# Kernel tuning notes

Measured on AMD Instinct MI355X. Metric: run time of the kernel, lower is better.

## Reference

```python
import jax, jax.numpy as jnp
import numpy as np

H = 128      # hidden_size
P = 50000    # num_predicates
C = 20000    # num_clauses
K = 3        # clause_size (3-SAT)
B = 4        # batch
SAT_ITERS = 2


def setup_inputs() -> dict:
    key = jax.random.key(0)
    ks = jax.random.split(key, 10)
    s = 0.02
    return {
        "clause_indices": jax.random.randint(ks[0], (B, C, K), 0, P),
        "variable_states": jax.random.normal(ks[1], (B, P, H), jnp.float32),
        "W_vc": jax.random.normal(ks[2], (H, H), jnp.float32) * s,
        "b_vc": jnp.zeros((H,), jnp.float32),
        "W_ce": jax.random.normal(ks[3], (H, H), jnp.float32) * s,
        "b_ce": jnp.zeros((H,), jnp.float32),
        "W_cv": jax.random.normal(ks[4], (H, H), jnp.float32) * s,
        "b_cv": jnp.zeros((H,), jnp.float32),
        "W_s1": jax.random.normal(ks[5], (H, H), jnp.float32) * s,
        "b_s1": jnp.zeros((H,), jnp.float32),
        "W_s2": jax.random.normal(ks[6], (1, H), jnp.float32) * s,
        "b_s2": jnp.zeros((1,), jnp.float32),
    }


def _forward(clause_indices, variable_states,
             W_vc, b_vc, W_ce, b_ce, W_cv, b_cv, W_s1, b_s1, W_s2, b_s2):
    Bn, Cn, Kn = clause_indices.shape
    Pn = variable_states.shape[1]
    # first-occurrence mask within each clause: duplicates of a variable inside
    # one clause must contribute once ((clause_indices == v).any(-1) semantics).
    eq = clause_indices[..., :, None] == clause_indices[..., None, :]  # [B,C,K,K]
    first = ~jnp.any(jnp.tril(eq, -1), axis=-1)                        # [B,C,K]
    w = first.reshape(-1).astype(variable_states.dtype)                # [B*C*K]
    flat_idx = clause_indices.reshape(-1)                              # [B*C*K]
    counts = jax.ops.segment_sum(w, flat_idx, num_segments=Pn)        # [P]
    batch_ix = jnp.arange(Bn)[:, None, None]

    for _ in range(SAT_ITERS):
        # clause side: gather -> var_to_clause -> mean over clause -> clause_embedding
        gathered = variable_states[batch_ix, clause_indices]           # [B,C,K,H]
        cv = jnp.einsum('bckh,oh->bcko', gathered, W_vc) + b_vc        # [B,C,K,H]
        clause_states = jnp.einsum('bch,oh->bco', cv.mean(2), W_ce) + b_ce  # [B,C,H]
        # variable side: per-variable mean of clause_to_var over all (b, c)
        # where the variable appears; message broadcast across batch.
        M = jnp.einsum('bch,oh->bco', clause_states, W_cv) + b_cv      # [B,C,H]
        Mflat = jnp.broadcast_to(M[:, :, None, :], (Bn, Cn, Kn, M.shape[-1])).reshape(-1, M.shape[-1])
        sums = jax.ops.segment_sum(Mflat * w[:, None], flat_idx, num_segments=Pn)  # [P,H]
        msgs = jnp.where(counts[:, None] > 0,
                         sums / jnp.maximum(counts, 1.0)[:, None],
                         0.0)                                          # [P,H]
        variable_states = variable_states + msgs[None]                 # broadcast over batch

    h = jax.nn.relu(jnp.einsum('bph,oh->bpo', variable_states, W_s1) + b_s1)
    logits = jnp.einsum('bph,oh->bpo', h, W_s2) + b_s2                 # [B,P,1]
    return jax.nn.sigmoid(logits)[..., 0]                              # [B,P]


def reference(clause_indices, variable_states,
              W_vc, b_vc, W_ce, b_ce, W_cv, b_cv, W_s1, b_s1, W_s2, b_s2):
    return _forward(clause_indices, variable_states,
                    W_vc, b_vc, W_ce, b_ce, W_cv, b_cv, W_s1, b_s1, W_s2, b_s2)
```

## Files before the change

kernel.cpp:

```cpp
#include <hip/hip_runtime.h>
#include <math.h>

using u16 = unsigned short;
using u32 = unsigned int;

namespace {
constexpr int Hdim = 128;
constexpr int Pn = 50000;
constexpr int Cn = 20000;
constexpr int Bn = 4;
constexpr int NClause = Bn * Cn;
constexpr int NRows = Bn * Pn;
constexpr int CAP = 64;
}

typedef __attribute__((ext_vector_type(4))) float f32x4;
typedef __attribute__((ext_vector_type(8))) short bf16x8;

static __device__ __forceinline__ float bf2f(u16 v) {
    u32 u = ((u32)v) << 16;
    return __builtin_bit_cast(float, u);
}
static __device__ __forceinline__ u16 f2bf(float f) {
    u32 u = __builtin_bit_cast(u32, f);
    u32 r = u + 0x7FFFu + ((u >> 16) & 1u);
    return (u16)(r >> 16);
}

__global__ __launch_bounds__(128) void setup_kernel(
    const float* __restrict__ W_vc, const float* __restrict__ b_vc,
    const float* __restrict__ W_ce, const float* __restrict__ b_ce,
    const float* __restrict__ W_cv, const float* __restrict__ b_cv,
    const float* __restrict__ W_s1,
    u16* __restrict__ WcombPack, u16* __restrict__ Ws1Pack,
    float* __restrict__ bias_comb, int* __restrict__ cursor) {
    int o = blockIdx.x, t = threadIdx.x;
    __shared__ float u[Hdim];
    __shared__ float red[Hdim];
    float acc = 0.f;
#pragma unroll 8
    for (int h = 0; h < Hdim; ++h) acc = fmaf(W_cv[o * Hdim + h], W_ce[h * Hdim + t], acc);
    u[t] = acc;
    float b1 = b_ce[t];
#pragma unroll 8
    for (int h = 0; h < Hdim; ++h) b1 = fmaf(W_ce[t * Hdim + h], b_vc[h], b1);
    red[t] = W_cv[o * Hdim + t] * b1;
    __syncthreads();
#pragma unroll
    for (int s = 64; s > 0; s >>= 1) {
        if (t < s) red[t] += red[t + s];
        __syncthreads();
    }
    if (t == 0) bias_comb[o] = red[0] + b_cv[o];
    float w = 0.f;
#pragma unroll 8
    for (int h = 0; h < Hdim; ++h) w = fmaf(u[h], W_vc[h * Hdim + t], w);
    int nt = o >> 4, ks = t >> 5, lofs = (t >> 3) & 3, j = t & 7;
    int lane = lofs * 16 + (o & 15);
    size_t dst = (size_t)(((nt * 4 + ks) * 64 + lane)) * 8 + j;
    WcombPack[dst] = f2bf(w);
    Ws1Pack[dst] = f2bf(W_s1[o * Hdim + t]);
    for (int i = o * 128 + t; i < Pn; i += 128 * 128) cursor[i] = 0;
}

__global__ void fill_kernel(const int* __restrict__ ci, int* __restrict__ cursor,
                            int* __restrict__ entries) {
    int fid = blockIdx.x * blockDim.x + threadIdx.x;
    if (fid >= NClause) return;
    int i0 = ci[fid * 3 + 0], i1 = ci[fid * 3 + 1], i2 = ci[fid * 3 + 2];
    int pos = atomicAdd(&cursor[i0], 1);
    entries[i0 * CAP + pos] = fid;
    if (i1 != i0) { pos = atomicAdd(&cursor[i1], 1); entries[i1 * CAP + pos] = fid; }
    if (i2 != i0 && i2 != i1) { pos = atomicAdd(&cursor[i2], 1); entries[i2 * CAP + pos] = fid; }
}

template <int FROM_F32>
__global__ __launch_bounds__(256) void clause_kernel(
    const int* __restrict__ ci, const float* __restrict__ vs0, const u16* __restrict__ msgs,
    const u16* __restrict__ Bpack, const float* __restrict__ bias, u16* __restrict__ M) {
    __shared__ __align__(16) u16 Atile[64 * 136];
    __shared__ __align__(16) u16 Btile[128 * 128];
    int tid = threadIdx.x;
    int block0 = blockIdx.x * 64;
    {
        const bf16x8* s = (const bf16x8*)Bpack;
        bf16x8* d = (bf16x8*)Btile;
#pragma unroll
        for (int i = 0; i < 8; ++i) d[tid + i * 256] = s[tid + i * 256];
    }
#pragma unroll
    for (int pass = 0; pass < 4; ++pass) {
        int t = pass * 256 + tid;
        int r = t >> 4, seg = t & 15;
        int fid = block0 + r;
        int i0 = ci[fid * 3 + 0], i1 = ci[fid * 3 + 1], i2 = ci[fid * 3 + 2];
        int co = seg * 8;
        float s[8];
        if (FROM_F32) {
            const float* base = vs0 + (size_t)(fid / Cn) * Pn * Hdim;
            const float* r0 = base + (size_t)i0 * Hdim + co;
            const float* r1 = base + (size_t)i1 * Hdim + co;
            const float* r2 = base + (size_t)i2 * Hdim + co;
            f32x4 a0 = *(const f32x4*)r0, a1 = *(const f32x4*)(r0 + 4);
            f32x4 b0 = *(const f32x4*)r1, b1 = *(const f32x4*)(r1 + 4);
            f32x4 c0 = *(const f32x4*)r2, c1 = *(const f32x4*)(r2 + 4);
#pragma unroll
            for (int j = 0; j < 4; ++j) {
                s[j] = a0[j] + b0[j] + c0[j];
                s[j + 4] = a1[j] + b1[j] + c1[j];
            }
        } else {
            bf16x8 v0 = *(const bf16x8*)(msgs + (size_t)i0 * Hdim + co);
            bf16x8 v1 = *(const bf16x8*)(msgs + (size_t)i1 * Hdim + co);
            bf16x8 v2 = *(const bf16x8*)(msgs + (size_t)i2 * Hdim + co);
#pragma unroll
            for (int j = 0; j < 8; ++j)
                s[j] = bf2f((u16)v0[j]) + bf2f((u16)v1[j]) + bf2f((u16)v2[j]);
        }
        bf16x8 o;
#pragma unroll
        for (int j = 0; j < 8; ++j) o[j] = (short)f2bf(s[j] * (1.f / 3.f));
        *(bf16x8*)(&Atile[r * 136 + seg * 8]) = o;
    }
    __syncthreads();
    int w = tid >> 6, l = tid & 63;
    int arow = w * 16 + (l & 15);
    int kofs = (l >> 4) * 8;
    f32x4 acc[8];
#pragma unroll
    for (int nt = 0; nt < 8; ++nt) acc[nt] = (f32x4){0.f, 0.f, 0.f, 0.f};
#pragma unroll
    for (int ks = 0; ks < 4; ++ks) {
        bf16x8 af = *(const bf16x8*)(&Atile[arow * 136 + ks * 32 + kofs]);
#pragma unroll
        for (int nt = 0; nt < 8; ++nt) {
            bf16x8 bfr = *(const bf16x8*)(&Btile[((nt * 4 + ks) * 64 + l) * 8]);
            acc[nt] = __builtin_amdgcn_mfma_f32_16x16x32_bf16(af, bfr, acc[nt], 0, 0, 0);
        }
    }
    __syncthreads();
    int crow = w * 16 + (l >> 4) * 4;
#pragma unroll
    for (int nt = 0; nt < 8; ++nt) {
        int col = nt * 16 + (l & 15);
        float bc = FROM_F32 ? bias[col] : 0.f;
#pragma unroll
        for (int reg = 0; reg < 4; ++reg)
            Atile[(crow + reg) * 136 + col] = f2bf(acc[nt][reg] + bc);
    }
    __syncthreads();
#pragma unroll
    for (int pass = 0; pass < 4; ++pass) {
        int t = pass * 256 + tid;
        int r = t >> 4, seg = t & 15;
        *(bf16x8*)(M + (size_t)(block0 + r) * Hdim + seg * 8) =
            *(const bf16x8*)(&Atile[r * 136 + seg * 8]);
    }
}

__global__ __launch_bounds__(256) void var_kernel(const u16* __restrict__ M,
                                                  const int* __restrict__ counts,
                                                  const int* __restrict__ entries,
                                                  u16* __restrict__ msgs, int iter2) {
    int wave = threadIdx.x >> 6, lane = threadIdx.x & 63;
    int p = blockIdx.x * 4 + wave;
    if (p >= Pn) return;
    int deg = counts[p];
    const int* ep = entries + p * CAP;
    float a0 = 0.f, a1 = 0.f;
    for (int e = 0; e < deg; ++e) {
        int cid = ep[e];
        u32 v = *(const u32*)(M + (size_t)cid * Hdim + lane * 2);
        a0 += bf2f((u16)(v & 0xffffu));
        a1 += bf2f((u16)(v >> 16));
    }
    if (deg > 0) { float inv = 1.f / (float)deg; a0 *= inv; a1 *= inv; }
    u32* mp = (u32*)(msgs + (size_t)p * Hdim + lane * 2);
    if (iter2) {
        u32 old = *mp;
        a0 += 2.f * bf2f((u16)(old & 0xffffu));
        a1 += 2.f * bf2f((u16)(old >> 16));
    }
    *mp = (u32)f2bf(a0) | ((u32)f2bf(a1) << 16);
}

__global__ __launch_bounds__(256) void final_kernel(
    const float* __restrict__ vs0, const u16* __restrict__ msgs, const u16* __restrict__ Bpack,
    const float* __restrict__ b_s1, const float* __restrict__ W_s2, const float* __restrict__ b_s2,
    float* __restrict__ out) {
    __shared__ __align__(16) u16 Atile[64 * 136];
    __shared__ __align__(16) u16 Btile[128 * 128];
    int tid = threadIdx.x;
    int block0 = blockIdx.x * 64;
    {
        const bf16x8* s = (const bf16x8*)Bpack;
        bf16x8* d = (bf16x8*)Btile;
#pragma unroll
        for (int i = 0; i < 8; ++i) d[tid + i * 256] = s[tid + i * 256];
    }
#pragma unroll
    for (int pass = 0; pass < 4; ++pass) {
        int t = pass * 256 + tid;
        int r = t >> 4, seg = t & 15;
        int row = block0 + r;
        int p = row % Pn;
        int co = seg * 8;
        const float* vp = vs0 + (size_t)row * Hdim + co;
        f32x4 x = *(const f32x4*)vp, y = *(const f32x4*)(vp + 4);
        bf16x8 m = *(const bf16x8*)(msgs + (size_t)p * Hdim + co);
        bf16x8 o;
#pragma unroll
        for (int j = 0; j < 4; ++j) {
            o[j] = (short)f2bf(x[j] + bf2f((u16)m[j]));
            o[j + 4] = (short)f2bf(y[j] + bf2f((u16)m[j + 4]));
        }
        *(bf16x8*)(&Atile[r * 136 + seg * 8]) = o;
    }
    __syncthreads();
    int w = tid >> 6, l = tid & 63;
    int arow = w * 16 + (l & 15);
    int kofs = (l >> 4) * 8;
    f32x4 acc[8];
#pragma unroll
    for (int nt = 0; nt < 8; ++nt) acc[nt] = (f32x4){0.f, 0.f, 0.f, 0.f};
#pragma unroll
    for (int ks = 0; ks < 4; ++ks) {
        bf16x8 af = *(const bf16x8*)(&Atile[arow * 136 + ks * 32 + kofs]);
#pragma unroll
        for (int nt = 0; nt < 8; ++nt) {
            bf16x8 bfr = *(const bf16x8*)(&Btile[((nt * 4 + ks) * 64 + l) * 8]);
            acc[nt] = __builtin_amdgcn_mfma_f32_16x16x32_bf16(af, bfr, acc[nt], 0, 0, 0);
        }
    }
    float part[4] = {0.f, 0.f, 0.f, 0.f};
#pragma unroll
    for (int nt = 0; nt < 8; ++nt) {
        int col = nt * 16 + (l & 15);
        float b1 = b_s1[col], w2 = W_s2[col];
#pragma unroll
        for (int reg = 0; reg < 4; ++reg)
            part[reg] += fmaxf(acc[nt][reg] + b1, 0.f) * w2;
    }
#pragma unroll
    for (int m = 1; m < 16; m <<= 1)
#pragma unroll
        for (int reg = 0; reg < 4; ++reg) part[reg] += __shfl_xor(part[reg], m, 64);
    if ((l & 15) == 0) {
        float lb = b_s2[0];
        int row0 = block0 + w * 16 + (l >> 4) * 4;
#pragma unroll
        for (int reg = 0; reg < 4; ++reg)
            out[row0 + reg] = 1.f / (1.f + expf(-(part[reg] + lb)));
    }
}

extern "C" void kernel_launch(void* const* d_in, const int* in_sizes, int n_in,
                              void* d_out, int out_size, void* d_ws, size_t ws_size,
                              hipStream_t stream) {
    (void)in_sizes; (void)n_in; (void)out_size; (void)ws_size;
    const int* ci = (const int*)d_in[0];
    const float* vs0 = (const float*)d_in[1];
    const float* W_vc = (const float*)d_in[2];
    const float* b_vc = (const float*)d_in[3];
    const float* W_ce = (const float*)d_in[4];
    const float* b_ce = (const float*)d_in[5];
    const float* W_cv = (const float*)d_in[6];
    const float* b_cv = (const float*)d_in[7];
    const float* W_s1 = (const float*)d_in[8];
    const float* b_s1 = (const float*)d_in[9];
    const float* W_s2 = (const float*)d_in[10];
    const float* b_s2 = (const float*)d_in[11];
    float* out = (float*)d_out;

    char* ws = (char*)d_ws;
    size_t off = 0;
    auto alloc = [&](size_t bytes) -> void* {
        off = (off + 255) & ~(size_t)255;
        void* p = ws + off;
        off += bytes;
        return p;
    };
    float* bias_comb = (float*)alloc(Hdim * 4);
    u16* WcombPack = (u16*)alloc(Hdim * Hdim * 2);
    u16* Ws1Pack = (u16*)alloc(Hdim * Hdim * 2);
    int* cursor = (int*)alloc(Pn * 4);
    int* entries = (int*)alloc((size_t)Pn * CAP * 4);
    u16* M = (u16*)alloc((size_t)NClause * Hdim * 2);
    u16* msgs = (u16*)alloc((size_t)Pn * Hdim * 2);

    setup_kernel<<<Hdim, Hdim, 0, stream>>>(W_vc, b_vc, W_ce, b_ce, W_cv, b_cv, W_s1,
                                            WcombPack, Ws1Pack, bias_comb, cursor);
    fill_kernel<<<(NClause + 255) / 256, 256, 0, stream>>>(ci, cursor, entries);

    clause_kernel<1><<<NClause / 64, 256, 0, stream>>>(ci, vs0, nullptr, WcombPack, bias_comb, M);
    var_kernel<<<(Pn + 3) / 4, 256, 0, stream>>>(M, cursor, entries, msgs, 0);
    clause_kernel<0><<<NClause / 64, 256, 0, stream>>>(ci, nullptr, msgs, WcombPack, bias_comb, M);
    var_kernel<<<(Pn + 3) / 4, 256, 0, stream>>>(M, cursor, entries, msgs, 1);
    final_kernel<<<NRows / 64, 256, 0, stream>>>(vs0, msgs, Ws1Pack, b_s1, W_s2, b_s2, out);
}
```

Baseline: 159.5 us.

## Fuse adjacency fill into first clause kernel, unroll var gather, persistent final kernel

Removes the separate fill_kernel by building the variable-to-clause adjacency lists inside the first clause kernel, using the first 64 threads of each block. The var_kernel gather loop is unrolled by two with separate accumulators so more loads are in flight at once. The final kernel becomes a grid-stride persistent kernel with 768 blocks, so the 128x128 weight tile is loaded into shared memory once per block instead of once per 64-row tile. These trade one fewer launch and less redundant weight loading for extra atomic work in the clause kernel and extra syncs per tile in the final kernel.

```diff
diff --git a/kernel.cpp b/kernel.cpp
--- a/kernel.cpp
+++ b/kernel.cpp
@@ -63,21 +63,11 @@
     for (int i = o * 128 + t; i < Pn; i += 128 * 128) cursor[i] = 0;
 }
 
-__global__ void fill_kernel(const int* __restrict__ ci, int* __restrict__ cursor,
-                            int* __restrict__ entries) {
-    int fid = blockIdx.x * blockDim.x + threadIdx.x;
-    if (fid >= NClause) return;
-    int i0 = ci[fid * 3 + 0], i1 = ci[fid * 3 + 1], i2 = ci[fid * 3 + 2];
-    int pos = atomicAdd(&cursor[i0], 1);
-    entries[i0 * CAP + pos] = fid;
-    if (i1 != i0) { pos = atomicAdd(&cursor[i1], 1); entries[i1 * CAP + pos] = fid; }
-    if (i2 != i0 && i2 != i1) { pos = atomicAdd(&cursor[i2], 1); entries[i2 * CAP + pos] = fid; }
-}
-
-template <int FROM_F32>
+template <int FROM_F32, int DO_FILL>
 __global__ __launch_bounds__(256) void clause_kernel(
     const int* __restrict__ ci, const float* __restrict__ vs0, const u16* __restrict__ msgs,
-    const u16* __restrict__ Bpack, const float* __restrict__ bias, u16* __restrict__ M) {
+    const u16* __restrict__ Bpack, const float* __restrict__ bias, u16* __restrict__ M,
+    int* __restrict__ cursor, int* __restrict__ entries) {
     __shared__ __align__(16) u16 Atile[64 * 136];
     __shared__ __align__(16) u16 Btile[128 * 128];
     int tid = threadIdx.x;
@@ -87,6 +77,14 @@
         bf16x8* d = (bf16x8*)Btile;
 #pragma unroll
         for (int i = 0; i < 8; ++i) d[tid + i * 256] = s[tid + i * 256];
+    }
+    if (DO_FILL && tid < 64) {
+        int fid = block0 + tid;
+        int i0 = ci[fid * 3 + 0], i1 = ci[fid * 3 + 1], i2 = ci[fid * 3 + 2];
+        int pos = atomicAdd(&cursor[i0], 1);
+        entries[i0 * CAP + pos] = fid;
+        if (i1 != i0) { pos = atomicAdd(&cursor[i1], 1); entries[i1 * CAP + pos] = fid; }
+        if (i2 != i0 && i2 != i1) { pos = atomicAdd(&cursor[i2], 1); entries[i2 * CAP + pos] = fid; }
     }
 #pragma unroll
     for (int pass = 0; pass < 4; ++pass) {
@@ -167,13 +165,23 @@
     if (p >= Pn) return;
     int deg = counts[p];
     const int* ep = entries + p * CAP;
-    float a0 = 0.f, a1 = 0.f;
-    for (int e = 0; e < deg; ++e) {
-        int cid = ep[e];
-        u32 v = *(const u32*)(M + (size_t)cid * Hdim + lane * 2);
+    float a0 = 0.f, a1 = 0.f, c0 = 0.f, c1 = 0.f;
+    int e = 0;
+    for (; e + 1 < deg; e += 2) {
+        int cidA = ep[e], cidB = ep[e + 1];
+        u32 vA = *(const u32*)(M + (size_t)cidA * Hdim + lane * 2);
+        u32 vB = *(const u32*)(M + (size_t)cidB * Hdim + lane * 2);
+        a0 += bf2f((u16)(vA & 0xffffu));
+        a1 += bf2f((u16)(vA >> 16));
+        c0 += bf2f((u16)(vB & 0xffffu));
+        c1 += bf2f((u16)(vB >> 16));
+    }
+    if (e < deg) {
+        u32 v = *(const u32*)(M + (size_t)ep[e] * Hdim + lane * 2);
         a0 += bf2f((u16)(v & 0xffffu));
         a1 += bf2f((u16)(v >> 16));
     }
+    a0 += c0; a1 += c1;
     if (deg > 0) { float inv = 1.f / (float)deg; a0 *= inv; a1 *= inv; }
     u32* mp = (u32*)(msgs + (size_t)p * Hdim + lane * 2);
     if (iter2) {
@@ -187,70 +195,73 @@
 __global__ __launch_bounds__(256) void final_kernel(
     const float* __restrict__ vs0, const u16* __restrict__ msgs, const u16* __restrict__ Bpack,
     const float* __restrict__ b_s1, const float* __restrict__ W_s2, const float* __restrict__ b_s2,
-    float* __restrict__ out) {
+    float* __restrict__ out, int ntiles) {
     __shared__ __align__(16) u16 Atile[64 * 136];
     __shared__ __align__(16) u16 Btile[128 * 128];
     int tid = threadIdx.x;
-    int block0 = blockIdx.x * 64;
     {
         const bf16x8* s = (const bf16x8*)Bpack;
         bf16x8* d = (bf16x8*)Btile;
 #pragma unroll
         for (int i = 0; i < 8; ++i) d[tid + i * 256] = s[tid + i * 256];
     }
-#pragma unroll
-    for (int pass = 0; pass < 4; ++pass) {
-        int t = pass * 256 + tid;
-        int r = t >> 4, seg = t & 15;
-        int row = block0 + r;
-        int p = row % Pn;
-        int co = seg * 8;
-        const float* vp = vs0 + (size_t)row * Hdim + co;
-        f32x4 x = *(const f32x4*)vp, y = *(const f32x4*)(vp + 4);
-        bf16x8 m = *(const bf16x8*)(msgs + (size_t)p * Hdim + co);
-        bf16x8 o;
-#pragma unroll
-        for (int j = 0; j < 4; ++j) {
-            o[j] = (short)f2bf(x[j] + bf2f((u16)m[j]));
-            o[j + 4] = (short)f2bf(y[j] + bf2f((u16)m[j + 4]));
-        }
-        *(bf16x8*)(&Atile[r * 136 + seg * 8]) = o;
-    }
-    __syncthreads();
     int w = tid >> 6, l = tid & 63;
     int arow = w * 16 + (l & 15);
     int kofs = (l >> 4) * 8;
-    f32x4 acc[8];
-#pragma unroll
-    for (int nt = 0; nt < 8; ++nt) acc[nt] = (f32x4){0.f, 0.f, 0.f, 0.f};
-#pragma unroll
-    for (int ks = 0; ks < 4; ++ks) {
-        bf16x8 af = *(const bf16x8*)(&Atile[arow * 136 + ks * 32 + kofs]);
+    for (int tile = blockIdx.x; tile < ntiles; tile += gridDim.x) {
+        __syncthreads();
+        int block0 = tile * 64;
+#pragma unroll
+        for (int pass = 0; pass < 4; ++pass) {
+            int t = pass * 256 + tid;
+            int r = t >> 4, seg = t & 15;
+            int row = block0 + r;
+            int p = row % Pn;
+            int co = seg * 8;
+            const float* vp = vs0 + (size_t)row * Hdim + co;
+            f32x4 x = *(const f32x4*)vp, y = *(const f32x4*)(vp + 4);
+            bf16x8 m = *(const bf16x8*)(msgs + (size_t)p * Hdim + co);
+            bf16x8 o;
+#pragma unroll
+            for (int j = 0; j < 4; ++j) {
+                o[j] = (short)f2bf(x[j] + bf2f((u16)m[j]));
+                o[j + 4] = (short)f2bf(y[j] + bf2f((u16)m[j + 4]));
+            }
+            *(bf16x8*)(&Atile[r * 136 + seg * 8]) = o;
+        }
+        __syncthreads();
+        f32x4 acc[8];
+#pragma unroll
+        for (int nt = 0; nt < 8; ++nt) acc[nt] = (f32x4){0.f, 0.f, 0.f, 0.f};
+#pragma unroll
+        for (int ks = 0; ks < 4; ++ks) {
+            bf16x8 af = *(const bf16x8*)(&Atile[arow * 136 + ks * 32 + kofs]);
+#pragma unroll
+            for (int nt = 0; nt < 8; ++nt) {
+                bf16x8 bfr = *(const bf16x8*)(&Btile[((nt * 4 + ks) * 64 + l) * 8]);
+                acc[nt] = __builtin_amdgcn_mfma_f32_16x16x32_bf16(af, bfr, acc[nt], 0, 0, 0);
+            }
+        }
+        float part[4] = {0.f, 0.f, 0.f, 0.f};
 #pragma unroll
         for (int nt = 0; nt < 8; ++nt) {
-            bf16x8 bfr = *(const bf16x8*)(&Btile[((nt * 4 + ks) * 64 + l) * 8]);
-            acc[nt] = __builtin_amdgcn_mfma_f32_16x16x32_bf16(af, bfr, acc[nt], 0, 0, 0);
-        }
-    }
-    float part[4] = {0.f, 0.f, 0.f, 0.f};
-#pragma unroll
-    for (int nt = 0; nt < 8; ++nt) {
-        int col = nt * 16 + (l & 15);
-        float b1 = b_s1[col], w2 = W_s2[col];
-#pragma unroll
-        for (int reg = 0; reg < 4; ++reg)
-            part[reg] += fmaxf(acc[nt][reg] + b1, 0.f) * w2;
-    }
-#pragma unroll
-    for (int m = 1; m < 16; m <<= 1)
-#pragma unroll
-        for (int reg = 0; reg < 4; ++reg) part[reg] += __shfl_xor(part[reg], m, 64);
-    if ((l & 15) == 0) {
-        float lb = b_s2[0];
-        int row0 = block0 + w * 16 + (l >> 4) * 4;
-#pragma unroll
-        for (int reg = 0; reg < 4; ++reg)
-            out[row0 + reg] = 1.f / (1.f + expf(-(part[reg] + lb)));
+            int col = nt * 16 + (l & 15);
+            float b1 = b_s1[col], w2 = W_s2[col];
+#pragma unroll
+            for (int reg = 0; reg < 4; ++reg)
+                part[reg] += fmaxf(acc[nt][reg] + b1, 0.f) * w2;
+        }
+#pragma unroll
+        for (int m = 1; m < 16; m <<= 1)
+#pragma unroll
+            for (int reg = 0; reg < 4; ++reg) part[reg] += __shfl_xor(part[reg], m, 64);
+        if ((l & 15) == 0) {
+            float lb = b_s2[0];
+            int row0 = block0 + w * 16 + (l >> 4) * 4;
+#pragma unroll
+            for (int reg = 0; reg < 4; ++reg)
+                out[row0 + reg] = 1.f / (1.f + expf(-(part[reg] + lb)));
+        }
     }
 }
 
@@ -290,11 +301,12 @@
 
     setup_kernel<<<Hdim, Hdim, 0, stream>>>(W_vc, b_vc, W_ce, b_ce, W_cv, b_cv, W_s1,
                                             WcombPack, Ws1Pack, bias_comb, cursor);
-    fill_kernel<<<(NClause + 255) / 256, 256, 0, stream>>>(ci, cursor, entries);
-
-    clause_kernel<1><<<NClause / 64, 256, 0, stream>>>(ci, vs0, nullptr, WcombPack, bias_comb, M);
+    clause_kernel<1, 1><<<NClause / 64, 256, 0, stream>>>(ci, vs0, nullptr, WcombPack,
+                                                          bias_comb, M, cursor, entries);
     var_kernel<<<(Pn + 3) / 4, 256, 0, stream>>>(M, cursor, entries, msgs, 0);
-    clause_kernel<0><<<NClause / 64, 256, 0, stream>>>(ci, nullptr, msgs, WcombPack, bias_comb, M);
+    clause_kernel<0, 0><<<NClause / 64, 256, 0, stream>>>(ci, nullptr, msgs, WcombPack,
+                                                          bias_comb, M, cursor, entries);
     var_kernel<<<(Pn + 3) / 4, 256, 0, stream>>>(M, cursor, entries, msgs, 1);
-    final_kernel<<<NRows / 64, 256, 0, stream>>>(vs0, msgs, Ws1Pack, b_s1, W_s2, b_s2, out);
-}
+    final_kernel<<<768, 256, 0, stream>>>(vs0, msgs, Ws1Pack, b_s1, W_s2, b_s2, out,
+                                          NRows / 64);
+}
```

Result: faster. 135.4 us (-15.1%).
